# Kernel optimization log

Hardware: AMD Instinct MI355X
Metric: run time of the kernel (lower is better)

The kernel has to match this reference:

```python
import jax, jax.numpy as jnp
import numpy as np

N_HEAD = 4
GROUPS = 32
EPS = 1e-5


def group_norm(x, scale, bias):
    B, C, H, W = x.shape
    xg = x.reshape(B, GROUPS, C // GROUPS, H, W)
    mu = xg.mean(axis=(2, 3, 4), keepdims=True)
    var = xg.var(axis=(2, 3, 4), keepdims=True)
    xg = (xg - mu) * jax.lax.rsqrt(var + EPS)
    x = xg.reshape(B, C, H, W)
    return x * scale[None, :, None, None] + bias[None, :, None, None]


def setup_inputs() -> dict:
    key = jax.random.key(0)
    k0, k1, k2 = jax.random.split(key, 3)
    B, C, H, W = 2, 64, 64, 64
    x = jax.random.normal(k0, (B, C, H, W), dtype=jnp.float32)
    gn_scale = jnp.ones((C,), dtype=jnp.float32)
    gn_bias = jnp.zeros((C,), dtype=jnp.float32)
    w_qkv = jax.random.normal(k1, (3 * C, C), dtype=jnp.float32) * 0.05  # 1x1 conv, no bias
    w_out = jax.random.normal(k2, (C, C), dtype=jnp.float32) * 0.05     # 1x1 conv
    b_out = jnp.zeros((C,), dtype=jnp.float32)
    return {"x": x, "gn_scale": gn_scale, "gn_bias": gn_bias,
            "w_qkv": w_qkv, "w_out": w_out, "b_out": b_out}


def reference(x, gn_scale, gn_bias, w_qkv, w_out, b_out):
    B, C, H, W = x.shape
    head_dim = C // N_HEAD
    norm = group_norm(x, gn_scale, gn_bias)
    # 1x1 conv == channel matmul
    qkv = jnp.einsum('oc,bchw->bohw', w_qkv, norm)
    qkv = qkv.reshape(B, N_HEAD, head_dim * 3, H, W)
    q, k, v = jnp.split(qkv, 3, axis=2)  # each [B, n, head_dim, H, W]
    # full spatial attention scores, scaled by sqrt(channel) as in source
    attn = jnp.einsum('bnchw,bncyx->bnhwyx', q, k) / jnp.sqrt(jnp.float32(C))
    attn = jax.nn.softmax(attn.reshape(B, N_HEAD, H, W, H * W), axis=-1)
    attn = attn.reshape(B, N_HEAD, H, W, H, W)
    out = jnp.einsum('bnhwyx,bncyx->bnchw', attn, v).reshape(B, C, H, W)
    out = jnp.einsum('oc,bchw->bohw', w_out, out) + b_out[None, :, None, None]
    return out + x
```

## Files before the change

### kernel.cpp

```cpp
#include <hip/hip_runtime.h>
#include <hip/hip_bf16.h>

typedef __attribute__((ext_vector_type(8))) short short8;
typedef __attribute__((ext_vector_type(4))) float f32x4;
typedef __attribute__((ext_vector_type(16))) float f32x16;
typedef __attribute__((ext_vector_type(4))) unsigned short ushort4v;
typedef __attribute__((ext_vector_type(4))) unsigned int uint4v;

#define DEV static __device__ __forceinline__

DEV unsigned short f2bf(float f){
  unsigned u = __float_as_uint(f);
  u += 0x7fffu + ((u >> 16) & 1u);
  return (unsigned short)(u >> 16);
}

DEV unsigned pack2bf(float a, float b){
  __hip_bfloat162 h = __float22bfloat162_rn(make_float2(a, b));
  unsigned u;
  __builtin_memcpy(&u, &h, 4);
  return u;
}

#define QSCALE 0.180336880111f

__global__ __launch_bounds__(256) void gn_partial_k(const float* __restrict__ x,
                                                    float* __restrict__ gp){
  int blk = blockIdx.x;
  float4 v = ((const float4*)(x + (size_t)blk*1024))[threadIdx.x];
  float s = v.x+v.y+v.z+v.w;
  float q = v.x*v.x+v.y*v.y+v.z*v.z+v.w*v.w;
  #pragma unroll
  for (int off = 1; off < 64; off <<= 1){
    s += __shfl_xor(s, off);
    q += __shfl_xor(q, off);
  }
  __shared__ float red[8];
  int w = threadIdx.x >> 6;
  if ((threadIdx.x & 63) == 0){ red[w*2] = s; red[w*2+1] = q; }
  __syncthreads();
  if (threadIdx.x == 0){
    gp[blk*2+0] = red[0]+red[2]+red[4]+red[6];
    gp[blk*2+1] = red[1]+red[3]+red[5]+red[7];
  }
}

__global__ __launch_bounds__(256) void qkv_k(const float* __restrict__ x,
    const float* __restrict__ gp, const float* __restrict__ gsc,
    const float* __restrict__ gbi, const float* __restrict__ wq,
    unsigned short* __restrict__ q, unsigned short* __restrict__ k,
    unsigned short* __restrict__ v){
  int b  = blockIdx.x >> 7;
  int s0 = (blockIdx.x & 127) * 32;
  __shared__ float W[192][68];
  __shared__ float A[32][68];
  __shared__ float MS[32][2];
  int t = threadIdx.x;
  for (int i = t; i < 3072; i += 256){
    int o = i >> 4, c4 = (i & 15) * 4;
    *(float4*)&W[o][c4] = ((const float4*)wq)[i];
  }
  if (t < 32){
    float s = 0.f, ss = 0.f;
    #pragma unroll
    for (int i = 0; i < 8; ++i){
      const float* pp = gp + ((b*32 + t)*8 + i)*2;
      s += pp[0]; ss += pp[1];
    }
    float mean = s * (1.f/8192.f);
    MS[t][0] = mean;
    MS[t][1] = rsqrtf(ss * (1.f/8192.f) - mean*mean + 1e-5f);
  }
  __syncthreads();
  {
    int c  = t >> 2;
    int s8 = (t & 3) * 8;
    const float* px = x + ((size_t)b*64 + c)*4096 + s0 + s8;
    float4 v0 = *(const float4*)px;
    float4 v1 = *(const float4*)(px + 4);
    float sc = gsc[c] * MS[c>>1][1];
    float bi = gbi[c] - MS[c>>1][0] * sc;
    A[s8+0][c]=v0.x*sc+bi; A[s8+1][c]=v0.y*sc+bi; A[s8+2][c]=v0.z*sc+bi; A[s8+3][c]=v0.w*sc+bi;
    A[s8+4][c]=v1.x*sc+bi; A[s8+5][c]=v1.y*sc+bi; A[s8+6][c]=v1.z*sc+bi; A[s8+7][c]=v1.w*sc+bi;
  }
  __syncthreads();
  int sl = t >> 3, grp = t & 7;
  float acc[24];
  #pragma unroll
  for (int j = 0; j < 24; ++j) acc[j] = 0.f;
  for (int c4 = 0; c4 < 16; ++c4){
    float4 a = *(const float4*)&A[sl][c4*4];
    #pragma unroll
    for (int j = 0; j < 24; ++j){
      float4 wv = *(const float4*)&W[grp + j*8][c4*4];
      acc[j] = fmaf(a.x, wv.x, fmaf(a.y, wv.y, fmaf(a.z, wv.z, fmaf(a.w, wv.w, acc[j]))));
    }
  }
  int s = s0 + sl;
  #pragma unroll
  for (int j = 0; j < 24; ++j){
    int o = grp + j*8;
    int n = o / 48, r = o % 48;
    size_t base = (((size_t)b*4 + n)*4096 + s)*16;
    float val = acc[j];
    if (r < 16)       q[base + r]      = f2bf(val * QSCALE);
    else if (r < 32)  k[base + r - 16] = f2bf(val);
    else              v[base + r - 32] = f2bf(val);
  }
}

template<int LNSP>
__global__ __launch_bounds__(256) void attn_k(const unsigned short* __restrict__ qb,
    const unsigned short* __restrict__ kb, const unsigned short* __restrict__ vb,
    float* __restrict__ part, float* __restrict__ lsums){
  constexpr int NSP = 1 << LNSP;
  constexpr int NT  = 64 >> LNSP;
  int blk = blockIdx.x;
  int bn = blk & 7;
  int sp = (blk >> 3) & (NSP - 1);
  int qt = blk >> (3 + LNSP);
  int t = threadIdx.x, w = t >> 6, l = t & 63;
  int lq = l & 31, hi = l >> 5;

  const unsigned short* Kp = kb + ((size_t)bn*4096 + sp*(NT*64))*16;
  const unsigned short* Vp = vb + ((size_t)bn*4096 + sp*(NT*64))*16;
  int qrow = qt*128 + w*32;
  const unsigned short* Qp = qb + ((size_t)bn*4096 + qrow)*16;

  __shared__ alignas(16) unsigned short Vt[2][32][72];
  for (int i = t; i < 2304; i += 256){
    int buf = (i >= 1152);
    int ii  = buf ? i - 1152 : i;
    int row = 16 + ii / 72, col = ii % 72;
    Vt[buf][row][col] = (row == 16) ? (unsigned short)0x3F80 : (unsigned short)0;
  }

  short8 qf = *(const short8*)(Qp + (size_t)lq*16 + hi*8);

  f32x16 O, zero;
  #pragma unroll
  for (int r = 0; r < 16; ++r){ O[r] = 0.f; zero[r] = 0.f; }

  int skv = t >> 2, sd = (t & 3) * 4;
  int xk = skv & 15;
  int scol = (skv & 48) + (xk & 3) + (((xk >> 2) & 1) << 3) + (((xk >> 3) & 1) << 2);
  const unsigned short* vsrc = Vp + (size_t)skv*16 + sd;
  const unsigned short* kaddr = Kp + (size_t)lq*16 + hi*8;

  short8 kf0 = *(const short8*)(kaddr);
  short8 kf1 = *(const short8*)(kaddr + 512);
  ushort4v vv = *(const ushort4v*)(vsrc);

  for (int kt = 0; kt < NT; ++kt){
    int cur = kt & 1;
    Vt[cur][sd+0][scol]=vv[0]; Vt[cur][sd+1][scol]=vv[1];
    Vt[cur][sd+2][scol]=vv[2]; Vt[cur][sd+3][scol]=vv[3];
    __syncthreads();

    bool pf = (kt + 1) < NT;
    short8 kn0 = {}, kn1 = {};
    ushort4v vn = {};
    if (pf){
      const unsigned short* ka = kaddr + (size_t)(kt+1)*1024;
      kn0 = *(const short8*)(ka);
      kn1 = *(const short8*)(ka + 512);
      vn  = *(const ushort4v*)(vsrc + (size_t)(kt+1)*1024);
    }

    f32x16 sA = __builtin_amdgcn_mfma_f32_32x32x16_bf16(kf0, qf, zero, 0, 0, 0);
    f32x16 sB = __builtin_amdgcn_mfma_f32_32x32x16_bf16(kf1, qf, zero, 0, 0, 0);

    #pragma unroll
    for (int r = 0; r < 16; ++r) sA[r] = __builtin_amdgcn_exp2f(sA[r]);
    #pragma unroll
    for (int r = 0; r < 16; ++r) sB[r] = __builtin_amdgcn_exp2f(sB[r]);

    auto pvstep = [&](const f32x16& pc, int h8, int vcol){
      uint4v pw;
      pw[0] = pack2bf(pc[h8+0], pc[h8+1]);
      pw[1] = pack2bf(pc[h8+2], pc[h8+3]);
      pw[2] = pack2bf(pc[h8+4], pc[h8+5]);
      pw[3] = pack2bf(pc[h8+6], pc[h8+7]);
      short8 pa = __builtin_bit_cast(short8, pw);
      short8 vf = *(const short8*)(&Vt[cur][lq][vcol + hi*8]);
      O = __builtin_amdgcn_mfma_f32_32x32x16_bf16(pa, vf, O, 0, 0, 0);
    };
    pvstep(sA, 0, 0);
    pvstep(sA, 8, 16);
    pvstep(sB, 0, 32);
    pvstep(sB, 8, 48);

    kf0 = kn0; kf1 = kn1; vv = vn;
  }

  float* Op = part + (((size_t)sp*8 + bn)*4096 + qrow)*16;
  size_t lbase = ((size_t)sp*8 + bn)*4096 + qrow;
  #pragma unroll
  for (int r = 0; r < 16; ++r){
    int qr = (r&3) + 8*(r>>2) + 4*hi;
    if (lq < 16) __builtin_nontemporal_store(O[r], &Op[(size_t)qr*16 + lq]);
  }
  if (lq == 16){
    #pragma unroll
    for (int r = 0; r < 16; ++r){
      int qr = (r&3) + 8*(r>>2) + 4*hi;
      __builtin_nontemporal_store(O[r], &lsums[lbase + qr]);
    }
  }
}

__global__ __launch_bounds__(256) void oproj_k(const float* __restrict__ part,
    const float* __restrict__ lsums, const float* __restrict__ wo,
    const float* __restrict__ bo, const float* __restrict__ x,
    float* __restrict__ out, int nsplit){
  int b  = blockIdx.x >> 8;
  int s0 = (blockIdx.x & 255) * 16;
  __shared__ float W[64][68];
  __shared__ float A[16][68];
  int t = threadIdx.x;
  for (int i = t; i < 1024; i += 256){
    int o = i >> 4, c4 = (i & 15) * 4;
    *(float4*)&W[o][c4] = ((const float4*)wo)[i];
  }
  {
    int sl = t & 15;
    int u  = t >> 4;
    int n = u >> 2, d4 = (u & 3) * 4;
    size_t row = ((size_t)b*4 + n)*4096 + s0 + sl;
    float L = 0.f;
    for (int sp = 0; sp < nsplit; ++sp)
      L += __builtin_nontemporal_load(&lsums[(size_t)sp*32768 + row]);
    f32x4 acc = {0.f,0.f,0.f,0.f};
    for (int sp = 0; sp < nsplit; ++sp){
      f32x4 u0 = __builtin_nontemporal_load(
          (const f32x4*)(part + ((size_t)sp*32768 + row)*16 + d4));
      acc += u0;
    }
    float inv = 1.f / L;
    A[sl][n*16+d4+0] = acc[0]*inv; A[sl][n*16+d4+1] = acc[1]*inv;
    A[sl][n*16+d4+2] = acc[2]*inv; A[sl][n*16+d4+3] = acc[3]*inv;
  }
  __syncthreads();
  int sl = t & 15, grp = t >> 4;
  float acc[4] = {0.f,0.f,0.f,0.f};
  for (int c4 = 0; c4 < 16; ++c4){
    float4 a = *(const float4*)&A[sl][c4*4];
    #pragma unroll
    for (int j = 0; j < 4; ++j){
      float4 wv = *(const float4*)&W[grp + j*16][c4*4];
      acc[j] = fmaf(a.x, wv.x, fmaf(a.y, wv.y, fmaf(a.z, wv.z, fmaf(a.w, wv.w, acc[j]))));
    }
  }
  int s = s0 + sl;
  #pragma unroll
  for (int j = 0; j < 4; ++j){
    int o = grp + j*16;
    size_t idx = ((size_t)b*64 + o)*4096 + s;
    out[idx] = acc[j] + bo[o] + x[idx];
  }
}

extern "C" void kernel_launch(void* const* d_in, const int* in_sizes, int n_in,
                              void* d_out, int out_size, void* d_ws, size_t ws_size,
                              hipStream_t stream){
  const float* x   = (const float*)d_in[0];
  const float* gsc = (const float*)d_in[1];
  const float* gbi = (const float*)d_in[2];
  const float* wq  = (const float*)d_in[3];
  const float* wo  = (const float*)d_in[4];
  const float* bo  = (const float*)d_in[5];
  float* out = (float*)d_out;

  char* ws = (char*)d_ws;
  float* gp         = (float*)ws;
  unsigned short* q = (unsigned short*)(ws + 8192);
  unsigned short* k = (unsigned short*)(ws + 8192 + 1048576);
  unsigned short* v = (unsigned short*)(ws + 8192 + 2097152);
  float* part       = (float*)(ws + 8192 + 3145728);

  size_t need8 = 8192 + 3145728 + 8u*2097152 + 8u*131072;
  bool big = ws_size >= need8;
  int nsplit = big ? 8 : 4;
  float* lsums = (float*)(ws + 8192 + 3145728 + (size_t)nsplit*2097152);

  gn_partial_k<<<512,  256, 0, stream>>>(x, gp);
  qkv_k       <<<256,  256, 0, stream>>>(x, gp, gsc, gbi, wq, q, k, v);
  if (big) attn_k<3><<<2048, 256, 0, stream>>>(q, k, v, part, lsums);
  else     attn_k<2><<<1024, 256, 0, stream>>>(q, k, v, part, lsums);
  oproj_k     <<<512,  256, 0, stream>>>(part, lsums, wo, bo, x, out, nsplit);
}
```

Before: 60.70 us.

## Pre-transpose V in qkv kernel and drop LDS staging in attention

```diff
diff --git a/kernel.cpp b/kernel.cpp
--- a/kernel.cpp
+++ b/kernel.cpp
@@ -4,7 +4,6 @@
 typedef __attribute__((ext_vector_type(8))) short short8;
 typedef __attribute__((ext_vector_type(4))) float f32x4;
 typedef __attribute__((ext_vector_type(16))) float f32x16;
-typedef __attribute__((ext_vector_type(4))) unsigned short ushort4v;
 typedef __attribute__((ext_vector_type(4))) unsigned int uint4v;
 
 #define DEV static __device__ __forceinline__
@@ -23,6 +22,8 @@
 }
 
 #define QSCALE 0.180336880111f
+#define NSPLIT 4
+#define NT 16
 
 __global__ __launch_bounds__(256) void gn_partial_k(const float* __restrict__ x,
                                                     float* __restrict__ gp){
@@ -49,7 +50,7 @@
     const float* __restrict__ gp, const float* __restrict__ gsc,
     const float* __restrict__ gbi, const float* __restrict__ wq,
     unsigned short* __restrict__ q, unsigned short* __restrict__ k,
-    unsigned short* __restrict__ v){
+    unsigned short* __restrict__ vt){
   int b  = blockIdx.x >> 7;
   int s0 = (blockIdx.x & 127) * 32;
   __shared__ float W[192][68];
@@ -70,6 +71,10 @@
     float mean = s * (1.f/8192.f);
     MS[t][0] = mean;
     MS[t][1] = rsqrtf(ss * (1.f/8192.f) - mean*mean + 1e-5f);
+  }
+  if (t < 128){
+    int n = t >> 5, si = t & 31;
+    vt[((size_t)(b*4 + n)*32 + 16)*4096 + s0 + si] = (unsigned short)0x3F80;
   }
   __syncthreads();
   {
@@ -97,74 +102,64 @@
     }
   }
   int s = s0 + sl;
+  int slp = (sl & 0x13) | (((sl >> 2) & 1) << 3) | (((sl >> 3) & 1) << 2);
   #pragma unroll
   for (int j = 0; j < 24; ++j){
     int o = grp + j*8;
     int n = o / 48, r = o % 48;
-    size_t base = (((size_t)b*4 + n)*4096 + s)*16;
     float val = acc[j];
-    if (r < 16)       q[base + r]      = f2bf(val * QSCALE);
-    else if (r < 32)  k[base + r - 16] = f2bf(val);
-    else              v[base + r - 32] = f2bf(val);
-  }
-}
-
-template<int LNSP>
+    if (r < 16){
+      q[((((size_t)b*4 + n)*4096 + s))*16 + r] = f2bf(val * QSCALE);
+    } else if (r < 32){
+      k[((((size_t)b*4 + n)*4096 + s))*16 + r - 16] = f2bf(val);
+    } else {
+      vt[((size_t)(b*4 + n)*32 + (r - 32))*4096 + s0 + slp] = f2bf(val);
+    }
+  }
+}
+
 __global__ __launch_bounds__(256) void attn_k(const unsigned short* __restrict__ qb,
-    const unsigned short* __restrict__ kb, const unsigned short* __restrict__ vb,
+    const unsigned short* __restrict__ kb, const unsigned short* __restrict__ vt,
     float* __restrict__ part, float* __restrict__ lsums){
-  constexpr int NSP = 1 << LNSP;
-  constexpr int NT  = 64 >> LNSP;
   int blk = blockIdx.x;
   int bn = blk & 7;
-  int sp = (blk >> 3) & (NSP - 1);
-  int qt = blk >> (3 + LNSP);
+  int sp = (blk >> 3) & (NSPLIT - 1);
+  int qt = blk >> 5;
   int t = threadIdx.x, w = t >> 6, l = t & 63;
   int lq = l & 31, hi = l >> 5;
 
   const unsigned short* Kp = kb + ((size_t)bn*4096 + sp*(NT*64))*16;
-  const unsigned short* Vp = vb + ((size_t)bn*4096 + sp*(NT*64))*16;
+  int vrow = (lq < 16) ? lq : 16;
+  const unsigned short* Vr = vt + ((size_t)bn*32 + vrow)*4096 + sp*(NT*64) + hi*8;
   int qrow = qt*128 + w*32;
   const unsigned short* Qp = qb + ((size_t)bn*4096 + qrow)*16;
 
-  __shared__ alignas(16) unsigned short Vt[2][32][72];
-  for (int i = t; i < 2304; i += 256){
-    int buf = (i >= 1152);
-    int ii  = buf ? i - 1152 : i;
-    int row = 16 + ii / 72, col = ii % 72;
-    Vt[buf][row][col] = (row == 16) ? (unsigned short)0x3F80 : (unsigned short)0;
-  }
-
   short8 qf = *(const short8*)(Qp + (size_t)lq*16 + hi*8);
+  const unsigned short* kaddr = Kp + (size_t)lq*16 + hi*8;
 
   f32x16 O, zero;
   #pragma unroll
   for (int r = 0; r < 16; ++r){ O[r] = 0.f; zero[r] = 0.f; }
-
-  int skv = t >> 2, sd = (t & 3) * 4;
-  int xk = skv & 15;
-  int scol = (skv & 48) + (xk & 3) + (((xk >> 2) & 1) << 3) + (((xk >> 3) & 1) << 2);
-  const unsigned short* vsrc = Vp + (size_t)skv*16 + sd;
-  const unsigned short* kaddr = Kp + (size_t)lq*16 + hi*8;
 
   short8 kf0 = *(const short8*)(kaddr);
   short8 kf1 = *(const short8*)(kaddr + 512);
-  ushort4v vv = *(const ushort4v*)(vsrc);
+  short8 vf0 = *(const short8*)(Vr);
+  short8 vf1 = *(const short8*)(Vr + 16);
+  short8 vf2 = *(const short8*)(Vr + 32);
+  short8 vf3 = *(const short8*)(Vr + 48);
 
   for (int kt = 0; kt < NT; ++kt){
-    int cur = kt & 1;
-    Vt[cur][sd+0][scol]=vv[0]; Vt[cur][sd+1][scol]=vv[1];
-    Vt[cur][sd+2][scol]=vv[2]; Vt[cur][sd+3][scol]=vv[3];
-    __syncthreads();
-
     bool pf = (kt + 1) < NT;
-    short8 kn0 = {}, kn1 = {};
-    ushort4v vn = {};
+    short8 kn0 = {}, kn1 = {}, vn0 = {}, vn1 = {}, vn2 = {}, vn3 = {};
     if (pf){
       const unsigned short* ka = kaddr + (size_t)(kt+1)*1024;
       kn0 = *(const short8*)(ka);
       kn1 = *(const short8*)(ka + 512);
-      vn  = *(const ushort4v*)(vsrc + (size_t)(kt+1)*1024);
+      const unsigned short* va = Vr + (size_t)(kt+1)*64;
+      vn0 = *(const short8*)(va);
+      vn1 = *(const short8*)(va + 16);
+      vn2 = *(const short8*)(va + 32);
+      vn3 = *(const short8*)(va + 48);
     }
 
     f32x16 sA = __builtin_amdgcn_mfma_f32_32x32x16_bf16(kf0, qf, zero, 0, 0, 0);
@@ -175,22 +170,22 @@
     #pragma unroll
     for (int r = 0; r < 16; ++r) sB[r] = __builtin_amdgcn_exp2f(sB[r]);
 
-    auto pvstep = [&](const f32x16& pc, int h8, int vcol){
+    auto pvstep = [&](const f32x16& pc, int h8, short8 vf){
       uint4v pw;
       pw[0] = pack2bf(pc[h8+0], pc[h8+1]);
       pw[1] = pack2bf(pc[h8+2], pc[h8+3]);
       pw[2] = pack2bf(pc[h8+4], pc[h8+5]);
       pw[3] = pack2bf(pc[h8+6], pc[h8+7]);
       short8 pa = __builtin_bit_cast(short8, pw);
-      short8 vf = *(const short8*)(&Vt[cur][lq][vcol + hi*8]);
       O = __builtin_amdgcn_mfma_f32_32x32x16_bf16(pa, vf, O, 0, 0, 0);
     };
-    pvstep(sA, 0, 0);
-    pvstep(sA, 8, 16);
-    pvstep(sB, 0, 32);
-    pvstep(sB, 8, 48);
-
-    kf0 = kn0; kf1 = kn1; vv = vn;
+    pvstep(sA, 0, vf0);
+    pvstep(sA, 8, vf1);
+    pvstep(sB, 0, vf2);
+    pvstep(sB, 8, vf3);
+
+    kf0 = kn0; kf1 = kn1;
+    vf0 = vn0; vf1 = vn1; vf2 = vn2; vf3 = vn3;
   }
 
   float* Op = part + (((size_t)sp*8 + bn)*4096 + qrow)*16;
@@ -212,7 +207,7 @@
 __global__ __launch_bounds__(256) void oproj_k(const float* __restrict__ part,
     const float* __restrict__ lsums, const float* __restrict__ wo,
     const float* __restrict__ bo, const float* __restrict__ x,
-    float* __restrict__ out, int nsplit){
+    float* __restrict__ out){
   int b  = blockIdx.x >> 8;
   int s0 = (blockIdx.x & 255) * 16;
   __shared__ float W[64][68];
@@ -228,10 +223,12 @@
     int n = u >> 2, d4 = (u & 3) * 4;
     size_t row = ((size_t)b*4 + n)*4096 + s0 + sl;
     float L = 0.f;
-    for (int sp = 0; sp < nsplit; ++sp)
+    #pragma unroll
+    for (int sp = 0; sp < NSPLIT; ++sp)
       L += __builtin_nontemporal_load(&lsums[(size_t)sp*32768 + row]);
     f32x4 acc = {0.f,0.f,0.f,0.f};
-    for (int sp = 0; sp < nsplit; ++sp){
+    #pragma unroll
+    for (int sp = 0; sp < NSPLIT; ++sp){
       f32x4 u0 = __builtin_nontemporal_load(
           (const f32x4*)(part + ((size_t)sp*32768 + row)*16 + d4));
       acc += u0;
@@ -272,20 +269,15 @@
   float* out = (float*)d_out;
 
   char* ws = (char*)d_ws;
-  float* gp         = (float*)ws;
-  unsigned short* q = (unsigned short*)(ws + 8192);
-  unsigned short* k = (unsigned short*)(ws + 8192 + 1048576);
-  unsigned short* v = (unsigned short*)(ws + 8192 + 2097152);
-  float* part       = (float*)(ws + 8192 + 3145728);
-
-  size_t need8 = 8192 + 3145728 + 8u*2097152 + 8u*131072;
-  bool big = ws_size >= need8;
-  int nsplit = big ? 8 : 4;
-  float* lsums = (float*)(ws + 8192 + 3145728 + (size_t)nsplit*2097152);
+  float* gp          = (float*)ws;
+  unsigned short* q  = (unsigned short*)(ws + 8192);
+  unsigned short* k  = (unsigned short*)(ws + 8192 + 1048576);
+  unsigned short* vt = (unsigned short*)(ws + 8192 + 2097152);
+  float* part        = (float*)(ws + 8192 + 4194304);
+  float* lsums       = (float*)(ws + 8192 + 4194304 + 8388608);
 
   gn_partial_k<<<512,  256, 0, stream>>>(x, gp);
-  qkv_k       <<<256,  256, 0, stream>>>(x, gp, gsc, gbi, wq, q, k, v);
-  if (big) attn_k<3><<<2048, 256, 0, stream>>>(q, k, v, part, lsums);
-  else     attn_k<2><<<1024, 256, 0, stream>>>(q, k, v, part, lsums);
-  oproj_k     <<<512,  256, 0, stream>>>(part, lsums, wo, bo, x, out, nsplit);
-}
+  qkv_k       <<<256,  256, 0, stream>>>(x, gp, gsc, gbi, wq, q, k, vt);
+  attn_k      <<<1024, 256, 0, stream>>>(q, k, vt, part, lsums);
+  oproj_k     <<<512,  256, 0, stream>>>(part, lsums, wo, bo, x, out);
+}
```

Result: faster. 55.68 us (-8.3%).
